# Kernel tuning notes

Measured on AMD Instinct MI355X. Metric: run time of the kernel, lower is better.

## Reference

```python
import jax, jax.numpy as jnp
import numpy as np

WIRE_DIM = 32
NUM_WIRES = 64
BATCH = 8192


def setup_inputs() -> dict:
    key = jax.random.key(0)
    k1, k2, k3, k4 = jax.random.split(key, 4)
    outputs = jax.random.normal(k1, (BATCH, NUM_WIRES * WIRE_DIM), dtype=jnp.float32)
    tests = jax.random.randint(k2, (BATCH, 2), 0, NUM_WIRES, dtype=jnp.int64)
    W1 = jax.random.normal(k3, (2 * WIRE_DIM, 10), dtype=jnp.float32) * 0.1
    b1 = jnp.zeros((10,), dtype=jnp.float32)
    W2 = jax.random.normal(k4, (10, 1), dtype=jnp.float32) * 0.1
    b2 = jnp.zeros((1,), dtype=jnp.float32)
    return {"outputs": outputs, "tests": tests, "W1": W1, "b1": b1, "W2": W2, "b2": b2}


def reference(outputs, tests, W1, b1, W2, b2):
    B = outputs.shape[0]
    W = outputs.shape[1] // WIRE_DIM          # num_wires
    wires = outputs.reshape(B, W, WIRE_DIM)   # [B, W, D]
    person = tests[:, 0]
    location = tests[:, 1]
    # gather_nd equivalent: person wire vector per batch element
    person_vec = wires[jnp.arange(B), person]                 # [B, D]
    # per-wire concat [person_vec, wire_vec] -> shared tiny MLP, vectorized over wires
    x = jnp.concatenate(
        [jnp.broadcast_to(person_vec[:, None, :], (B, W, WIRE_DIM)), wires], axis=-1
    )                                                          # [B, W, 2D]
    h = jax.nn.relu(jnp.einsum("bwd,dh->bwh", x, W1) + b1)     # [B, W, 10]
    logits = (jnp.einsum("bwh,ho->bwo", h, W2) + b2)[..., 0]   # [B, W]
    # sparse softmax cross entropy with location labels
    loss = -jnp.take_along_axis(jax.nn.log_softmax(logits, axis=-1),
                                location[:, None], axis=-1)[:, 0]  # [B]
    return loss
```

## Files before the change

kernel.cpp:

```cpp
#include <hip/hip_runtime.h>

#define WIRE_DIM  32
#define NUM_WIRES 64
#define BATCH     8192
#define HID       10
#define STRIDE    36

__device__ __forceinline__ float rl(float x, int slane) {
    return __uint_as_float(__builtin_amdgcn_readlane(__float_as_uint(x), slane));
}

__global__ __launch_bounds__(256) void isnet_kernel(
    const float* __restrict__ outputs,
    const int*   __restrict__ tests,
    const float* __restrict__ W1,
    const float* __restrict__ bias1,
    const float* __restrict__ W2,
    const float* __restrict__ bias2,
    float*       __restrict__ out)
{
    __shared__ __align__(16) float stage[4][NUM_WIRES * STRIDE];

    const int tid  = threadIdx.x;
    const int lane = tid & 63;
    const int wave = tid >> 6;
    float* buf = stage[wave];

    const int b = blockIdx.x * 4 + wave;

    const int sp = __builtin_amdgcn_readfirstlane(tests[2 * b]);
    const int sl = __builtin_amdgcn_readfirstlane(tests[2 * b + 1]);

    const float* g = outputs + (size_t)b * (NUM_WIRES * WIRE_DIM) + lane * 4;
    const int r  = lane >> 3;
    const int cc = lane & 7;
    {
        float4 c[8];
        #pragma unroll
        for (int t = 0; t < 8; ++t) c[t] = *(const float4*)(g + t * 256);
        #pragma unroll
        for (int t = 0; t < 8; ++t)
            *(float4*)&buf[(t * 8 + r) * STRIDE + cc * 4] = c[t];
    }

    float4 x[8], p[8];
    #pragma unroll
    for (int t = 0; t < 8; ++t)
        x[t] = *(const float4*)&buf[lane * STRIDE + t * 4];
    #pragma unroll
    for (int t = 0; t < 8; ++t)
        p[t] = *(const float4*)&buf[sp * STRIDE + t * 4];

    float acc[HID];
    #pragma unroll
    for (int h = 0; h < HID; ++h) acc[h] = bias1[h];

    #pragma unroll
    for (int j = 0; j < 8; ++j) {
        const float* wp = W1 + (4 * j) * HID;
        const float* ww = W1 + (32 + 4 * j) * HID;
        #pragma unroll
        for (int h = 0; h < HID; ++h) {
            acc[h] += p[j].x * wp[0 * HID + h] + p[j].y * wp[1 * HID + h]
                    + p[j].z * wp[2 * HID + h] + p[j].w * wp[3 * HID + h]
                    + x[j].x * ww[0 * HID + h] + x[j].y * ww[1 * HID + h]
                    + x[j].z * ww[2 * HID + h] + x[j].w * ww[3 * HID + h];
        }
    }

    float v = bias2[0];
    #pragma unroll
    for (int h = 0; h < HID; ++h) v += fmaxf(acc[h], 0.f) * W2[h];

    float m = v;
    #pragma unroll
    for (int off = 32; off > 0; off >>= 1) m = fmaxf(m, __shfl_xor(m, off));
    float s = __expf(v - m);
    #pragma unroll
    for (int off = 32; off > 0; off >>= 1) s += __shfl_xor(s, off);
    float lv = rl(v, sl);
    if (lane == 0) out[b] = m + __logf(s) - lv;
}

extern "C" void kernel_launch(void* const* d_in, const int* in_sizes, int n_in,
                              void* d_out, int out_size, void* d_ws, size_t ws_size,
                              hipStream_t stream) {
    const float* outputs = (const float*)d_in[0];
    const int*   tests   = (const int*)d_in[1];
    const float* W1      = (const float*)d_in[2];
    const float* b1      = (const float*)d_in[3];
    const float* W2      = (const float*)d_in[4];
    const float* b2      = (const float*)d_in[5];
    float* out = (float*)d_out;

    isnet_kernel<<<BATCH / 4, 256, 0, stream>>>(
        outputs, tests, W1, b1, W2, b2, out);
}
```

Before: 103.9 us.

## Stage wire rows in two half-width LDS passes to cut shared memory and registers

```diff
diff --git a/kernel.cpp b/kernel.cpp
--- a/kernel.cpp
+++ b/kernel.cpp
@@ -4,13 +4,13 @@
 #define NUM_WIRES 64
 #define BATCH     8192
 #define HID       10
-#define STRIDE    36
+#define HSTRIDE   20
 
 __device__ __forceinline__ float rl(float x, int slane) {
     return __uint_as_float(__builtin_amdgcn_readlane(__float_as_uint(x), slane));
 }
 
-__global__ __launch_bounds__(256) void isnet_kernel(
+__global__ __launch_bounds__(256, 8) void isnet_kernel(
     const float* __restrict__ outputs,
     const int*   __restrict__ tests,
     const float* __restrict__ W1,
@@ -19,7 +19,7 @@
     const float* __restrict__ bias2,
     float*       __restrict__ out)
 {
-    __shared__ __align__(16) float stage[4][NUM_WIRES * STRIDE];
+    __shared__ __align__(16) float stage[4][NUM_WIRES * HSTRIDE];
 
     const int tid  = threadIdx.x;
     const int lane = tid & 63;
@@ -32,39 +32,40 @@
     const int sl = __builtin_amdgcn_readfirstlane(tests[2 * b + 1]);
 
     const float* g = outputs + (size_t)b * (NUM_WIRES * WIRE_DIM) + lane * 4;
-    const int r  = lane >> 3;
-    const int cc = lane & 7;
-    {
-        float4 c[8];
-        #pragma unroll
-        for (int t = 0; t < 8; ++t) c[t] = *(const float4*)(g + t * 256);
-        #pragma unroll
-        for (int t = 0; t < 8; ++t)
-            *(float4*)&buf[(t * 8 + r) * STRIDE + cc * 4] = c[t];
-    }
+    float4 c[8];
+    #pragma unroll
+    for (int t = 0; t < 8; ++t) c[t] = *(const float4*)(g + t * 256);
 
-    float4 x[8], p[8];
-    #pragma unroll
-    for (int t = 0; t < 8; ++t)
-        x[t] = *(const float4*)&buf[lane * STRIDE + t * 4];
-    #pragma unroll
-    for (int t = 0; t < 8; ++t)
-        p[t] = *(const float4*)&buf[sp * STRIDE + t * 4];
+    const int r0   = lane >> 3;
+    const int cpos = (lane & 3) * 4;
+    const bool loA = (lane & 7) < 4;
 
     float acc[HID];
     #pragma unroll
     for (int h = 0; h < HID; ++h) acc[h] = bias1[h];
 
     #pragma unroll
-    for (int j = 0; j < 8; ++j) {
-        const float* wp = W1 + (4 * j) * HID;
-        const float* ww = W1 + (32 + 4 * j) * HID;
-        #pragma unroll
-        for (int h = 0; h < HID; ++h) {
-            acc[h] += p[j].x * wp[0 * HID + h] + p[j].y * wp[1 * HID + h]
-                    + p[j].z * wp[2 * HID + h] + p[j].w * wp[3 * HID + h]
-                    + x[j].x * ww[0 * HID + h] + x[j].y * ww[1 * HID + h]
-                    + x[j].z * ww[2 * HID + h] + x[j].w * ww[3 * HID + h];
+    for (int pass = 0; pass < 2; ++pass) {
+        if (loA == (pass == 0)) {
+            #pragma unroll
+            for (int t = 0; t < 8; ++t)
+                *(float4*)&buf[(t * 8 + r0) * HSTRIDE + cpos] = c[t];
+        }
+
+        #pragma unroll 1
+        for (int jj = 0; jj < 4; ++jj) {
+            float4 x = *(const float4*)&buf[lane * HSTRIDE + jj * 4];
+            float4 p = *(const float4*)&buf[sp   * HSTRIDE + jj * 4];
+            const int j = pass * 4 + jj;
+            const float* wp = W1 + (4 * j) * HID;
+            const float* ww = W1 + (32 + 4 * j) * HID;
+            #pragma unroll
+            for (int h = 0; h < HID; ++h) {
+                acc[h] += p.x * wp[0 * HID + h] + p.y * wp[1 * HID + h]
+                        + p.z * wp[2 * HID + h] + p.w * wp[3 * HID + h]
+                        + x.x * ww[0 * HID + h] + x.y * ww[1 * HID + h]
+                        + x.z * ww[2 * HID + h] + x.w * ww[3 * HID + h];
+            }
         }
     }
 
```

Measured after the change: 106.1 us. 2.1% more time.
